# Performance work log

Measured on AMD Instinct MI355X. Metric: run time of the kernel, lower is better.

The kernel has to match this reference:

```python
import jax, jax.numpy as jnp
import numpy as np
from jax import lax

N, L, LQ = 1024, 120, 30
V, D = 50000, 200
POSV, P = 201, 5
H, R = 230, 96
BAG = 8
B = N // BAG
EMB = 3 * D + 2 * P  # 610


def setup_inputs() -> dict:
    key = jax.random.key(0)
    k = jax.random.split(key, 14)
    X = jax.random.randint(k[0], (N, L), 0, V, dtype=jnp.int32)
    Q = jax.random.randint(k[1], (N, LQ), 0, V, dtype=jnp.int32)
    X_Pos1 = jax.random.randint(k[2], (N, L), 0, POSV, dtype=jnp.int32)
    X_Pos2 = jax.random.randint(k[3], (N, L), 0, POSV, dtype=jnp.int32)
    starts = jnp.arange(B, dtype=jnp.int32) * BAG
    X_Scope = jnp.stack([starts, starts + BAG], axis=1)  # [B,2] bag boundaries
    X_Rel = jax.random.randint(k[4], (B,), 0, R, dtype=jnp.int32)
    word_emb = jax.random.normal(k[5], (V, D), jnp.float32) * 0.02
    pos1_emb = jax.random.normal(k[6], (POSV, P), jnp.float32) * 0.02
    pos2_emb = jax.random.normal(k[7], (POSV, P), jnp.float32) * 0.02
    ws_w = jax.random.normal(k[8], (D,), jnp.float32) * 0.05
    wq_w = jax.random.normal(k[9], (D,), jnp.float32) * 0.05
    wsq_w = jax.random.normal(k[10], (D,), jnp.float32) * 0.05
    conv_w = jax.random.normal(k[11], (H, EMB, 3), jnp.float32) * 0.02
    rel_w = jax.random.normal(k[12], (R, H), jnp.float32) * 0.05
    return {
        'X': X, 'Q': Q, 'X_Pos1': X_Pos1, 'X_Pos2': X_Pos2,
        'X_Scope': X_Scope, 'X_Rel': X_Rel,
        'word_emb': word_emb, 'pos1_emb': pos1_emb, 'pos2_emb': pos2_emb,
        'ws_w': ws_w, 'ws_b': jnp.zeros((), jnp.float32),
        'wq_w': wq_w, 'wq_b': jnp.zeros((), jnp.float32),
        'wsq_w': wsq_w, 'wsq_b': jnp.zeros((), jnp.float32),
        'conv_w': conv_w, 'conv_b': jnp.zeros((H,), jnp.float32),
        'rel_w': rel_w, 'rel_b': jnp.zeros((R,), jnp.float32),
    }


def _forward(X, Q, X_Pos1, X_Pos2, X_Scope, X_Rel, word_emb, pos1_emb, pos2_emb,
             ws_w, ws_b, wq_w, wq_b, wsq_w, wsq_b, conv_w, conv_b, rel_w, rel_b):
    s = word_emb[X]            # [N,L,D]
    q = word_emb[Q]            # [N,LQ,D]
    p1 = pos1_emb[X_Pos1]      # [N,L,P]
    p2 = pos2_emb[X_Pos2]
    # ---- qs_att (BiDAF-style), vectorized over the original per-q-position loop ----
    sq = jnp.einsum('nld,nqd,d->nlq', s, q, wsq_w) + wsq_b            # [N,L,LQ]
    h = (s @ ws_w + ws_b)[:, :, None] + (q @ wq_w + wq_b)[:, None, :] + sq
    a = jax.nn.softmax(h, axis=2)
    s2q = jnp.einsum('nlq,nqd->nld', a, q)                            # s2q_att
    bvec = jax.nn.softmax(jnp.max(h, axis=2), axis=1)                 # [N,L]
    q2s = jnp.einsum('nl,nld->nd', bvec, s)[:, None, :]               # [N,1,D]
    x = jnp.concatenate([s, s * s2q, s * q2s], axis=-1)               # [N,L,3D]
    x = jnp.concatenate([x, p1, p2], axis=-1)                         # [N,L,EMB]
    # ---- CNN encoder: conv1d(k=3, same) -> max-over-time -> relu ----
    xc = lax.conv_general_dilated(x.transpose(0, 2, 1), conv_w, (1,), 'SAME',
                                  dimension_numbers=('NCH', 'OIH', 'NCH'))
    xc = xc + conv_b[None, :, None]
    feat = jax.nn.relu(jnp.max(xc, axis=2))                           # [N,H]
    # ---- bag self-attention: per-bag scaled dot-product over sentences ----
    bag_id = jnp.searchsorted(X_Scope[:, 1], jnp.arange(feat.shape[0]), side='right')
    same = bag_id[:, None] == bag_id[None, :]
    scores = (feat @ feat.T) / jnp.sqrt(jnp.float32(feat.shape[-1]))
    scores = jnp.where(same, scores, -1e30)
    feat = jax.nn.softmax(scores, axis=-1) @ feat                     # [N,H]
    # ---- selective attention with gold relation query (segment softmax) ----
    relq = rel_w[X_Rel]                                               # [B,H]
    z = jnp.einsum('nh,nh->n', feat, relq[bag_id])
    m = jax.ops.segment_max(z, bag_id, num_segments=B)
    e = jnp.exp(z - m[bag_id])
    denom = jax.ops.segment_sum(e, bag_id, num_segments=B)
    w = e / denom[bag_id]
    bag_rep = jax.ops.segment_sum(w[:, None] * feat, bag_id, num_segments=B)
    return bag_rep @ rel_w.T + rel_b                                  # [B,R]


def reference(X, Q, X_Pos1, X_Pos2, X_Scope, X_Rel, word_emb, pos1_emb, pos2_emb,
              ws_w, ws_b, wq_w, wq_b, wsq_w, wsq_b, conv_w, conv_b, rel_w, rel_b):
    return _forward(X, Q, X_Pos1, X_Pos2, X_Scope, X_Rel, word_emb, pos1_emb, pos2_emb,
                    ws_w, ws_b, wq_w, wq_b, wsq_w, wsq_b, conv_w, conv_b, rel_w, rel_b)
```

## Files before the change

### kernel.cpp

```cpp
#include <hip/hip_runtime.h>
#include <hip/hip_bf16.h>

#define N_    1024
#define L_    120
#define LQ_   30
#define D_    200
#define P_    5
#define H_    230
#define R_    96
#define BAG_  8
#define B_    128
#define EMB_  610
#define SROWS 130
#define SSTR  232
#define XSTR  40
#define NCH   21

typedef __hip_bfloat16 bf16;
typedef __attribute__((ext_vector_type(8))) short short8;
typedef __attribute__((ext_vector_type(4))) short short4_;
typedef __attribute__((ext_vector_type(4))) float f32x4;

__device__ __forceinline__ float wred_sum64(float v) {
#pragma unroll
  for (int m = 32; m; m >>= 1) v += __shfl_xor(v, m, 64);
  return v;
}
__device__ __forceinline__ float wred_max64(float v) {
#pragma unroll
  for (int m = 32; m; m >>= 1) v = fmaxf(v, __shfl_xor(v, m, 64));
  return v;
}
__device__ __forceinline__ short f2b(float f) {
  bf16 h = __float2bfloat16(f);
  return __builtin_bit_cast(short, h);
}
__device__ __forceinline__ float b2f(bf16 h) { return __bfloat162float(h); }

__global__ __launch_bounds__(256) void k0_prep_w(
    const float* __restrict__ conv_w, bf16* __restrict__ wt)
{
  const int idx = blockIdx.x * 256 + threadIdx.x;
  int e = idx & 7, lane = (idx >> 3) & 63;
  int fid = idx >> 9;
  int ni = fid & 15, cb = (fid >> 4) % NCH, k = fid / (NCH * 16);
  int h = ni * 16 + (lane & 15);
  int ccl = ((lane >> 4) << 3) + e;
  float v = 0.f;
  if (h < H_) {
    int emb_c = -1;
    if (cb < 7) {
      int d = cb * 32 + ccl;
      if (d < D_) emb_c = d;
    } else if (cb < 20) {
      int t = cb - 7;
      int d = 16 * t + (ccl & 15);
      if (d < D_) emb_c = (ccl < 16) ? (D_ + d) : (2 * D_ + d);
    } else if (ccl < 2 * P_) {
      emb_c = 3 * D_ + ccl;
    }
    if (emb_c >= 0) v = conv_w[(size_t)h * (EMB_ * 3) + emb_c * 3 + k];
  }
  wt[idx] = __float2bfloat16(v);
}

__global__ __launch_bounds__(512, 2) void kf_fused(
    const int* __restrict__ X, const int* __restrict__ Q,
    const int* __restrict__ P1, const int* __restrict__ P2,
    const float* __restrict__ word_emb,
    const float* __restrict__ pos1_emb, const float* __restrict__ pos2_emb,
    const float* __restrict__ ws_w, const float* __restrict__ ws_b,
    const float* __restrict__ wq_w, const float* __restrict__ wq_b,
    const float* __restrict__ wsq_w,
    const bf16* __restrict__ wt, const float* __restrict__ conv_b,
    float* __restrict__ feat)
{
  const int n = blockIdx.x;
  const int tid = threadIdx.x;
  const int w = tid >> 6, lane = tid & 63;
  const int g = lane >> 4, c = lane & 15;
  const int wm = w >> 2, wn = w & 3;

  __shared__ __align__(16) bf16 s_lds[SROWS][SSTR];
  __shared__ __align__(16) bf16 qT[208][40];
  __shared__ __align__(16) bf16 a_bf[128][40];
  __shared__ __align__(16) bf16 xstage[3][SROWS][XSTR];
  __shared__ __align__(16) bf16 pos_lds[L_][10];
  __shared__ float hred[8][64];
  __shared__ float wsv[D_], wqv[D_], wsqv[D_];
  __shared__ float sdot[128], qdot[32], hmax[128], bvec[L_];
  __shared__ float q2p[2][D_];
  __shared__ int xidxs[L_], qidxs[LQ_];

  bf16 (*qsw)[SSTR] = (bf16(*)[SSTR])xstage;

  {
    const int4 z4 = {0, 0, 0, 0};
    for (int t = tid; t < SROWS * SSTR * 2 / 16; t += 512) ((int4*)s_lds)[t] = z4;
    for (int t = tid; t < 208 * 40 * 2 / 16;     t += 512) ((int4*)qT)[t] = z4;
    for (int t = tid; t < 32 * SSTR * 2 / 16;    t += 512) ((int4*)qsw)[t] = z4;
  }
  if (tid < 2) qdot[30 + tid] = 0.f;
  if (tid >= 120 && tid < 128) sdot[tid] = 0.f;
  for (int t = tid; t < D_; t += 512) { wsv[t] = ws_w[t]; wqv[t] = wq_w[t]; wsqv[t] = wsq_w[t]; }
  if (tid < L_) xidxs[tid] = X[n * L_ + tid];
  else if (tid >= 128 && tid < 128 + LQ_) qidxs[tid - 128] = Q[n * LQ_ + (tid - 128)];
  __syncthreads();

  const float wsb = ws_b[0], wqb = wq_b[0];

#pragma unroll 5
  for (int l = w; l < L_; l += 8) {
    const int idx = xidxs[l];
    if (lane < 50) {
      const int d = lane * 4;
      float4 v = *(const float4*)(word_emb + (size_t)idx * D_ + d);
      short4_ pk; pk.x = f2b(v.x); pk.y = f2b(v.y); pk.z = f2b(v.z); pk.w = f2b(v.w);
      *(short4_*)&s_lds[1 + l][d] = pk;
    }
  }
  for (int e = tid; e < L_ * 10; e += 512) {
    int r = e / 10, p = e % 10;
    float v = (p < P_) ? pos1_emb[(size_t)P1[n * L_ + r] * P_ + p]
                       : pos2_emb[(size_t)P2[n * L_ + r] * P_ + (p - P_)];
    pos_lds[r][p] = __float2bfloat16(v);
  }
  for (int j = w; j < LQ_; j += 8) {
    const int idx = qidxs[j];
    float part = 0.f;
    if (lane < 50) {
      const int d = lane * 4;
      float4 v = *(const float4*)(word_emb + (size_t)idx * D_ + d);
      part = v.x * wqv[d] + v.y * wqv[d + 1] + v.z * wqv[d + 2] + v.w * wqv[d + 3];
      short4_ pk;
      pk.x = f2b(v.x * wsqv[d]);     pk.y = f2b(v.y * wsqv[d + 1]);
      pk.z = f2b(v.z * wsqv[d + 2]); pk.w = f2b(v.w * wsqv[d + 3]);
      *(short4_*)&qsw[j][d] = pk;
      qT[d][j]     = __float2bfloat16(v.x);
      qT[d + 1][j] = __float2bfloat16(v.y);
      qT[d + 2][j] = __float2bfloat16(v.z);
      qT[d + 3][j] = __float2bfloat16(v.w);
    }
    float sum = wred_sum64(part);
    if (lane == 0) qdot[j] = sum + wqb;
  }
  __syncthreads();

  if (tid < 480) {
    const int r = tid >> 2, base = (tid & 3) * 50;
    float a = 0.f;
#pragma unroll 5
    for (int i = 0; i < 50; i += 2) {
      a += b2f(s_lds[1 + r][base + i]) * wsv[base + i];
      a += b2f(s_lds[1 + r][base + i + 1]) * wsv[base + i + 1];
    }
    a += __shfl_xor(a, 1, 64);
    a += __shfl_xor(a, 2, 64);
    if ((tid & 3) == 0) sdot[r] = a + wsb;
  }
  __syncthreads();

  {
    f32x4 acc0 = {0.f, 0.f, 0.f, 0.f}, acc1 = {0.f, 0.f, 0.f, 0.f};
#pragma unroll
    for (int kk = 0; kk < 7; ++kk) {
      short8 af = *(const short8*)&s_lds[1 + 16 * w + c][kk * 32 + g * 8];
      short8 b0 = *(const short8*)&qsw[c][kk * 32 + g * 8];
      short8 b1 = *(const short8*)&qsw[16 + c][kk * 32 + g * 8];
      acc0 = __builtin_amdgcn_mfma_f32_16x16x32_bf16(af, b0, acc0, 0, 0, 0);
      acc1 = __builtin_amdgcn_mfma_f32_16x16x32_bf16(af, b1, acc1, 0, 0, 0);
    }
    const int rbase = 16 * w + 4 * g;
    const float qd0 = qdot[c], qd1 = qdot[16 + c];
#pragma unroll
    for (int reg = 0; reg < 4; ++reg) {
      const int r = rbase + reg;
      const float s0 = sdot[r];
      float h0 = acc0[reg] + s0 + qd0;
      float h1 = (c < 14) ? (acc1[reg] + s0 + qd1) : -1e30f;
      float m = fmaxf(h0, h1);
#pragma unroll
      for (int msk = 1; msk < 16; msk <<= 1) m = fmaxf(m, __shfl_xor(m, msk, 64));
      float e0 = expf(h0 - m);
      float e1 = (c < 14) ? expf(h1 - m) : 0.f;
      float ssum = e0 + e1;
#pragma unroll
      for (int msk = 1; msk < 16; msk <<= 1) ssum += __shfl_xor(ssum, msk, 64);
      float inv = 1.f / ssum;
      a_bf[r][c]      = __float2bfloat16(e0 * inv);
      a_bf[r][16 + c] = __float2bfloat16(e1 * inv);
      if (c == 0) hmax[r] = m;
    }
  }
  __syncthreads();

  if (w == 0) {
    float v0 = hmax[lane];
    float v1 = (lane < L_ - 64) ? hmax[64 + lane] : -1e30f;
    float m = wred_max64(fmaxf(v0, v1));
    float e0 = expf(v0 - m);
    float e1 = (lane < L_ - 64) ? expf(v1 - m) : 0.f;
    float inv = 1.f / wred_sum64(e0 + e1);
    bvec[lane] = e0 * inv;
    if (lane < L_ - 64) bvec[64 + lane] = e1 * inv;
  } else {
    const int4 z4 = {0, 0, 0, 0};
    for (int t = tid - 64; t < 3 * SROWS * XSTR * 2 / 16; t += 448) ((int4*)xstage)[t] = z4;
  }
  __syncthreads();
  {
    const int d = tid & 255, half = tid >> 8;
    if (d < D_) {
      const int lb = half * 60;
      float a0 = 0.f, a1 = 0.f, a2 = 0.f, a3 = 0.f;
      for (int l = 0; l < 60; l += 4) {
        a0 += bvec[lb + l]     * b2f(s_lds[1 + lb + l][d]);
        a1 += bvec[lb + l + 1] * b2f(s_lds[1 + lb + l + 1][d]);
        a2 += bvec[lb + l + 2] * b2f(s_lds[1 + lb + l + 2][d]);
        a3 += bvec[lb + l + 3] * b2f(s_lds[1 + lb + l + 3][d]);
      }
      q2p[half][d] = (a0 + a1) + (a2 + a3);
    }
  }
  __syncthreads();

  const short* wts = (const short*)wt;
  const short8 aft = *(const short8*)&a_bf[16 * w + c][g * 8];

  auto STAGE = [&](int t, bf16 (*buf)[XSTR]) {
    if (t < 13) {
      short8 bfr = *(const short8*)&qT[t * 16 + c][g * 8];
      f32x4 o = __builtin_amdgcn_mfma_f32_16x16x32_bf16(aft, bfr, (f32x4){0.f,0.f,0.f,0.f}, 0, 0, 0);
#pragma unroll
      for (int reg = 0; reg < 4; ++reg) {
        const int r = 16 * w + 4 * g + reg;
        if (r < L_) {
          float sv = b2f(s_lds[1 + r][t * 16 + c]);
          buf[1 + r][c] = __float2bfloat16(sv * o[reg]);
        }
      }
#pragma unroll
      for (int e = tid; e < L_ * 16; e += 512) {
        const int r = e >> 4, cc = e & 15, dd = t * 16 + cc;
        float v = (dd < D_) ? b2f(s_lds[1 + r][dd]) * (q2p[0][dd] + q2p[1][dd]) : 0.f;
        buf[1 + r][16 + cc] = __float2bfloat16(v);
      }
    } else {
#pragma unroll
      for (int e = tid; e < SROWS * 32; e += 512) {
        const int r = e >> 5, cc = e & 31;
        bf16 v = __float2bfloat16(0.f);
        if (r >= 1 && r <= L_ && cc < 2 * P_) v = pos_lds[r - 1][cc];
        buf[r][cc] = v;
      }
    }
  };

  f32x4 acc[4][4];
#pragma unroll
  for (int i = 0; i < 4; ++i)
#pragma unroll
    for (int j = 0; j < 4; ++j) acc[i][j] = (f32x4){0.f, 0.f, 0.f, 0.f};

  STAGE(0, xstage[0]);

  for (int t = 0; t < 14; ++t) {
    short8 bw[3][4];
#pragma unroll
    for (int k = 0; k < 3; ++k)
#pragma unroll
      for (int ni = 0; ni < 4; ++ni)
        bw[k][ni] = *(const short8*)(
            wts + (((size_t)((k * NCH + 7 + t) * 16 + wn * 4 + ni)) << 9) + lane * 8);

    if (t < 13) STAGE(t + 1, xstage[(t + 1) % 3]);

    if (t < 7) {
      short8 af[3][4];
#pragma unroll
      for (int k = 0; k < 3; ++k)
#pragma unroll
        for (int mi = 0; mi < 4; ++mi)
          af[k][mi] = *(const short8*)&s_lds[wm * 64 + mi * 16 + c + k][t * 32 + g * 8];
#pragma unroll
      for (int k = 0; k < 3; ++k)
#pragma unroll
        for (int ni = 0; ni < 4; ++ni) {
          const short8 b1 = *(const short8*)(
              wts + (((size_t)((k * NCH + t) * 16 + wn * 4 + ni)) << 9) + lane * 8);
#pragma unroll
          for (int mi = 0; mi < 4; ++mi)
            acc[mi][ni] = __builtin_amdgcn_mfma_f32_16x16x32_bf16(af[k][mi], b1, acc[mi][ni], 0, 0, 0);
        }
    }
    __syncthreads();

    {
      bf16 (*buf)[XSTR] = xstage[t % 3];
      short8 afx[3][4];
#pragma unroll
      for (int k = 0; k < 3; ++k)
#pragma unroll
        for (int mi = 0; mi < 4; ++mi)
          afx[k][mi] = *(const short8*)&buf[wm * 64 + mi * 16 + c + k][g * 8];
#pragma unroll
      for (int k = 0; k < 3; ++k)
#pragma unroll
        for (int ni = 0; ni < 4; ++ni)
#pragma unroll
          for (int mi = 0; mi < 4; ++mi)
            acc[mi][ni] = __builtin_amdgcn_mfma_f32_16x16x32_bf16(afx[k][mi], bw[k][ni], acc[mi][ni], 0, 0, 0);
    }
  }

  const int pbase = wm * 64 + (g << 2);
#pragma unroll
  for (int ni = 0; ni < 4; ++ni) {
    float m = -1e30f;
#pragma unroll
    for (int mi = 0; mi < 4; ++mi)
#pragma unroll
      for (int reg = 0; reg < 4; ++reg) {
        int pos = pbase + mi * 16 + reg;
        if (pos < L_) m = fmaxf(m, acc[mi][ni][reg]);
      }
    m = fmaxf(m, __shfl_xor(m, 16, 64));
    m = fmaxf(m, __shfl_xor(m, 32, 64));
    if (g == 0) hred[w][ni * 16 + c] = m;
  }
  __syncthreads();
  for (int h = tid; h < H_; h += 512) {
    int wn2 = h >> 6, hl = h & 63;
    float m = fmaxf(hred[wn2][hl], hred[wn2 + 4][hl]);
    feat[(size_t)n * H_ + h] = fmaxf(0.f, m + conv_b[h]);
  }
}

__global__ __launch_bounds__(256) void k3_bag(
    const float* __restrict__ feat, const int* __restrict__ X_Rel,
    const float* __restrict__ rel_w, const float* __restrict__ rel_b,
    float* __restrict__ out)
{
  const int b = blockIdx.x;
  const int tid = threadIdx.x;
  __shared__ float f[BAG_][231];
  __shared__ float f2[BAG_][231];
  __shared__ float sc[BAG_][BAG_];
  __shared__ float relq[H_];
  __shared__ float zred[BAG_];
  __shared__ float wsel[BAG_];
  __shared__ float brep[H_];

  for (int t = tid; t < BAG_ * H_; t += 256) {
    int i = t / H_, h = t % H_;
    f[i][h] = feat[(size_t)(b * BAG_ + i) * H_ + h];
  }
  const int rel = X_Rel[b];
  for (int t = tid; t < H_; t += 256) relq[t] = rel_w[(size_t)rel * H_ + t];
  __syncthreads();

  if (tid < BAG_ * BAG_) {
    int i = tid >> 3, j = tid & 7;
    float acc = 0.f;
    for (int h = 0; h < H_; ++h) acc += f[i][h] * f[j][h];
    sc[i][j] = acc * (1.0f / sqrtf((float)H_));
  }
  __syncthreads();
  if (tid < BAG_) {
    float m = -1e30f;
    for (int j = 0; j < BAG_; ++j) m = fmaxf(m, sc[tid][j]);
    float s = 0.f;
    for (int j = 0; j < BAG_; ++j) { float e = expf(sc[tid][j] - m); sc[tid][j] = e; s += e; }
    float inv = 1.0f / s;
    for (int j = 0; j < BAG_; ++j) sc[tid][j] *= inv;
  }
  __syncthreads();
  for (int t = tid; t < BAG_ * H_; t += 256) {
    int i = t / H_, h = t % H_;
    float acc = 0.f;
#pragma unroll
    for (int j = 0; j < BAG_; ++j) acc += sc[i][j] * f[j][h];
    f2[i][h] = acc;
  }
  __syncthreads();
  if (tid < BAG_) {
    float acc = 0.f;
    for (int h = 0; h < H_; ++h) acc += f2[tid][h] * relq[h];
    zred[tid] = acc;
  }
  __syncthreads();
  if (tid == 0) {
    float m = -1e30f;
    for (int i = 0; i < BAG_; ++i) m = fmaxf(m, zred[i]);
    float s = 0.f;
    for (int i = 0; i < BAG_; ++i) { float e = expf(zred[i] - m); wsel[i] = e; s += e; }
    float inv = 1.0f / s;
    for (int i = 0; i < BAG_; ++i) wsel[i] *= inv;
  }
  __syncthreads();
  for (int t = tid; t < H_; t += 256) {
    float acc = 0.f;
#pragma unroll
    for (int i = 0; i < BAG_; ++i) acc += wsel[i] * f2[i][t];
    brep[t] = acc;
  }
  __syncthreads();
  if (tid < R_) {
    float acc = 0.f;
    for (int h = 0; h < H_; ++h) acc += brep[h] * rel_w[(size_t)tid * H_ + h];
    out[(size_t)b * R_ + tid] = acc + rel_b[tid];
  }
}

extern "C" void kernel_launch(void* const* d_in, const int* in_sizes, int n_in,
                              void* d_out, int out_size, void* d_ws, size_t ws_size,
                              hipStream_t stream)
{
  const int*   X        = (const int*)d_in[0];
  const int*   Q        = (const int*)d_in[1];
  const int*   P1       = (const int*)d_in[2];
  const int*   P2       = (const int*)d_in[3];
  const int*   X_Rel    = (const int*)d_in[5];
  const float* word_emb = (const float*)d_in[6];
  const float* pos1_emb = (const float*)d_in[7];
  const float* pos2_emb = (const float*)d_in[8];
  const float* ws_w     = (const float*)d_in[9];
  const float* ws_b     = (const float*)d_in[10];
  const float* wq_w     = (const float*)d_in[11];
  const float* wq_b     = (const float*)d_in[12];
  const float* wsq_w    = (const float*)d_in[13];
  const float* conv_w   = (const float*)d_in[15];
  const float* conv_b   = (const float*)d_in[16];
  const float* rel_w    = (const float*)d_in[17];
  const float* rel_b    = (const float*)d_in[18];

  const size_t feat_bytes = ((size_t)N_ * H_ * sizeof(float) + 255) & ~(size_t)255;
  float* feat = (float*)d_ws;
  bf16*  wt   = (bf16*)((char*)d_ws + feat_bytes);

  const int wt_elems = 3 * NCH * 16 * 64 * 8;
  k0_prep_w<<<wt_elems / 256, 256, 0, stream>>>(conv_w, wt);
  kf_fused<<<N_, 512, 0, stream>>>(X, Q, P1, P2, word_emb, pos1_emb, pos2_emb,
                                   ws_w, ws_b, wq_w, wq_b, wsq_w, wt, conv_b, feat);
  k3_bag<<<B_, 256, 0, stream>>>(feat, X_Rel, rel_w, rel_b, (float*)d_out);
}
```

Measured before the change: 233.1 us.

## Double block to 1024 threads and restructure conv GEMM into paired chunk stages

The fused kernel now launches 1024 threads per block (16 waves) instead of 512 with two blocks per CU. The conv MFMA tiling changes from a 2x4 wave grid with 4 N-tiles each to a 2x8 grid with 2 N-tiles. Staging of the attention-derived x-chunks now prepares two chunks per iteration (one per wave-row half) into a wider double buffer, replacing the triple-buffered one-chunk pipeline. The sdot dot-product runs concurrently with the first MFMA phase on the spare waves. Intent is more waves per block and fewer barriers per chunk, at the cost of losing two-blocks-per-CU overlap and raising register pressure per thread.

```diff
diff --git a/kernel.cpp b/kernel.cpp
--- a/kernel.cpp
+++ b/kernel.cpp
@@ -13,7 +13,7 @@
 #define EMB_  610
 #define SROWS 130
 #define SSTR  232
-#define XSTR  40
+#define XSTR  72
 #define NCH   21
 
 typedef __hip_bfloat16 bf16;
@@ -64,7 +64,7 @@
   wt[idx] = __float2bfloat16(v);
 }
 
-__global__ __launch_bounds__(512, 2) void kf_fused(
+__global__ __launch_bounds__(1024, 1) void kf_fused(
     const int* __restrict__ X, const int* __restrict__ Q,
     const int* __restrict__ P1, const int* __restrict__ P2,
     const float* __restrict__ word_emb,
@@ -79,38 +79,39 @@
   const int tid = threadIdx.x;
   const int w = tid >> 6, lane = tid & 63;
   const int g = lane >> 4, c = lane & 15;
-  const int wm = w >> 2, wn = w & 3;
+  const int wm = w >> 3;
+  const int wn = w & 7;
+  const int w8 = w & 7;
 
   __shared__ __align__(16) bf16 s_lds[SROWS][SSTR];
   __shared__ __align__(16) bf16 qT[208][40];
   __shared__ __align__(16) bf16 a_bf[128][40];
-  __shared__ __align__(16) bf16 xstage[3][SROWS][XSTR];
+  __shared__ __align__(16) bf16 xstage[2][SROWS][XSTR];
   __shared__ __align__(16) bf16 pos_lds[L_][10];
-  __shared__ float hred[8][64];
+  __shared__ float hred[16][32];
   __shared__ float wsv[D_], wqv[D_], wsqv[D_];
   __shared__ float sdot[128], qdot[32], hmax[128], bvec[L_];
-  __shared__ float q2p[2][D_];
+  __shared__ float q2p[4][D_];
   __shared__ int xidxs[L_], qidxs[LQ_];
 
-  bf16 (*qsw)[SSTR] = (bf16(*)[SSTR])xstage;
+  bf16 (*qsw)[SSTR] = (bf16(*)[SSTR])&xstage[0][0][0];
 
   {
     const int4 z4 = {0, 0, 0, 0};
-    for (int t = tid; t < SROWS * SSTR * 2 / 16; t += 512) ((int4*)s_lds)[t] = z4;
-    for (int t = tid; t < 208 * 40 * 2 / 16;     t += 512) ((int4*)qT)[t] = z4;
-    for (int t = tid; t < 32 * SSTR * 2 / 16;    t += 512) ((int4*)qsw)[t] = z4;
+    for (int t = tid; t < SROWS * SSTR * 2 / 16; t += 1024) ((int4*)s_lds)[t] = z4;
+    for (int t = tid; t < 208 * 40 * 2 / 16;     t += 1024) ((int4*)qT)[t] = z4;
+    for (int t = tid; t < 32 * SSTR * 2 / 16;    t += 1024) ((int4*)qsw)[t] = z4;
   }
   if (tid < 2) qdot[30 + tid] = 0.f;
   if (tid >= 120 && tid < 128) sdot[tid] = 0.f;
-  for (int t = tid; t < D_; t += 512) { wsv[t] = ws_w[t]; wqv[t] = wq_w[t]; wsqv[t] = wsq_w[t]; }
+  for (int t = tid; t < D_; t += 1024) { wsv[t] = ws_w[t]; wqv[t] = wq_w[t]; wsqv[t] = wsq_w[t]; }
   if (tid < L_) xidxs[tid] = X[n * L_ + tid];
   else if (tid >= 128 && tid < 128 + LQ_) qidxs[tid - 128] = Q[n * LQ_ + (tid - 128)];
   __syncthreads();
 
   const float wsb = ws_b[0], wqb = wq_b[0];
 
-#pragma unroll 5
-  for (int l = w; l < L_; l += 8) {
+  for (int l = w; l < L_; l += 16) {
     const int idx = xidxs[l];
     if (lane < 50) {
       const int d = lane * 4;
@@ -119,13 +120,13 @@
       *(short4_*)&s_lds[1 + l][d] = pk;
     }
   }
-  for (int e = tid; e < L_ * 10; e += 512) {
+  for (int e = tid; e < L_ * 10; e += 1024) {
     int r = e / 10, p = e % 10;
     float v = (p < P_) ? pos1_emb[(size_t)P1[n * L_ + r] * P_ + p]
                        : pos2_emb[(size_t)P2[n * L_ + r] * P_ + (p - P_)];
     pos_lds[r][p] = __float2bfloat16(v);
   }
-  for (int j = w; j < LQ_; j += 8) {
+  for (int j = w; j < LQ_; j += 16) {
     const int idx = qidxs[j];
     float part = 0.f;
     if (lane < 50) {
@@ -146,22 +147,8 @@
   }
   __syncthreads();
 
-  if (tid < 480) {
-    const int r = tid >> 2, base = (tid & 3) * 50;
-    float a = 0.f;
-#pragma unroll 5
-    for (int i = 0; i < 50; i += 2) {
-      a += b2f(s_lds[1 + r][base + i]) * wsv[base + i];
-      a += b2f(s_lds[1 + r][base + i + 1]) * wsv[base + i + 1];
-    }
-    a += __shfl_xor(a, 1, 64);
-    a += __shfl_xor(a, 2, 64);
-    if ((tid & 3) == 0) sdot[r] = a + wsb;
-  }
-  __syncthreads();
-
-  {
-    f32x4 acc0 = {0.f, 0.f, 0.f, 0.f}, acc1 = {0.f, 0.f, 0.f, 0.f};
+  f32x4 acc0 = {0.f, 0.f, 0.f, 0.f}, acc1 = {0.f, 0.f, 0.f, 0.f};
+  if (w < 8) {
 #pragma unroll
     for (int kk = 0; kk < 7; ++kk) {
       short8 af = *(const short8*)&s_lds[1 + 16 * w + c][kk * 32 + g * 8];
@@ -170,6 +157,24 @@
       acc0 = __builtin_amdgcn_mfma_f32_16x16x32_bf16(af, b0, acc0, 0, 0, 0);
       acc1 = __builtin_amdgcn_mfma_f32_16x16x32_bf16(af, b1, acc1, 0, 0, 0);
     }
+  } else {
+    const int idx = tid - 512;
+    if (idx < 480) {
+      const int r = idx >> 2, base = (idx & 3) * 50;
+      float a = 0.f;
+#pragma unroll 5
+      for (int i = 0; i < 50; i += 2) {
+        a += b2f(s_lds[1 + r][base + i]) * wsv[base + i];
+        a += b2f(s_lds[1 + r][base + i + 1]) * wsv[base + i + 1];
+      }
+      a += __shfl_xor(a, 1, 64);
+      a += __shfl_xor(a, 2, 64);
+      if ((idx & 3) == 0) sdot[r] = a + wsb;
+    }
+  }
+  __syncthreads();
+
+  if (w < 8) {
     const int rbase = 16 * w + 4 * g;
     const float qd0 = qdot[c], qd1 = qdot[16 + c];
 #pragma unroll
@@ -191,6 +196,9 @@
       a_bf[r][16 + c] = __float2bfloat16(e1 * inv);
       if (c == 0) hmax[r] = m;
     }
+  } else {
+    const int4 z4 = {0, 0, 0, 0};
+    for (int t = tid - 512; t < 2 * SROWS * XSTR * 2 / 16; t += 512) ((int4*)xstage)[t] = z4;
   }
   __syncthreads();
 
@@ -203,119 +211,112 @@
     float inv = 1.f / wred_sum64(e0 + e1);
     bvec[lane] = e0 * inv;
     if (lane < L_ - 64) bvec[64 + lane] = e1 * inv;
-  } else {
-    const int4 z4 = {0, 0, 0, 0};
-    for (int t = tid - 64; t < 3 * SROWS * XSTR * 2 / 16; t += 448) ((int4*)xstage)[t] = z4;
-  }
-  __syncthreads();
+  }
+  __syncthreads();
+
   {
-    const int d = tid & 255, half = tid >> 8;
+    const int d = tid & 255, quarter = tid >> 8;
     if (d < D_) {
-      const int lb = half * 60;
-      float a0 = 0.f, a1 = 0.f, a2 = 0.f, a3 = 0.f;
-      for (int l = 0; l < 60; l += 4) {
+      const int lb = quarter * 30;
+      float a0 = 0.f, a1 = 0.f;
+      for (int l = 0; l < 30; l += 2) {
         a0 += bvec[lb + l]     * b2f(s_lds[1 + lb + l][d]);
         a1 += bvec[lb + l + 1] * b2f(s_lds[1 + lb + l + 1][d]);
-        a2 += bvec[lb + l + 2] * b2f(s_lds[1 + lb + l + 2][d]);
-        a3 += bvec[lb + l + 3] * b2f(s_lds[1 + lb + l + 3][d]);
-      }
-      q2p[half][d] = (a0 + a1) + (a2 + a3);
+      }
+      q2p[quarter][d] = a0 + a1;
     }
   }
   __syncthreads();
 
   const short* wts = (const short*)wt;
-  const short8 aft = *(const short8*)&a_bf[16 * w + c][g * 8];
-
-  auto STAGE = [&](int t, bf16 (*buf)[XSTR]) {
-    if (t < 13) {
-      short8 bfr = *(const short8*)&qT[t * 16 + c][g * 8];
-      f32x4 o = __builtin_amdgcn_mfma_f32_16x16x32_bf16(aft, bfr, (f32x4){0.f,0.f,0.f,0.f}, 0, 0, 0);
-#pragma unroll
-      for (int reg = 0; reg < 4; ++reg) {
-        const int r = 16 * w + 4 * g + reg;
-        if (r < L_) {
-          float sv = b2f(s_lds[1 + r][t * 16 + c]);
-          buf[1 + r][c] = __float2bfloat16(sv * o[reg]);
+  const short8 aft = *(const short8*)&a_bf[16 * w8 + c][g * 8];
+
+  f32x4 acc[4][2];
+#pragma unroll
+  for (int i = 0; i < 4; ++i) {
+    acc[i][0] = (f32x4){0.f, 0.f, 0.f, 0.f};
+    acc[i][1] = (f32x4){0.f, 0.f, 0.f, 0.f};
+  }
+
+  for (int p = 0; p < 7; ++p) {
+    short8 bw[2][3][2];
+#pragma unroll
+    for (int s2 = 0; s2 < 2; ++s2) {
+      const int t = 2 * p + s2;
+      const int cb = (t < 13) ? (7 + t) : 20;
+#pragma unroll
+      for (int k = 0; k < 3; ++k)
+#pragma unroll
+        for (int ni = 0; ni < 2; ++ni)
+          bw[s2][k][ni] = *(const short8*)(
+              wts + (((size_t)((k * NCH + cb) * 16 + wn * 2 + ni)) << 9) + lane * 8);
+    }
+
+    {
+      const int t = 2 * p + wm;
+      bf16 (*buf)[XSTR] = xstage[p & 1];
+      if (t < 13) {
+        short8 bfr = *(const short8*)&qT[t * 16 + c][g * 8];
+        f32x4 o = __builtin_amdgcn_mfma_f32_16x16x32_bf16(aft, bfr, (f32x4){0.f,0.f,0.f,0.f}, 0, 0, 0);
+#pragma unroll
+        for (int reg = 0; reg < 4; ++reg) {
+          const int r = 16 * w8 + 4 * g + reg;
+          if (r < L_) {
+            float sv = b2f(s_lds[1 + r][t * 16 + c]);
+            buf[1 + r][(t & 1) * 32 + c] = __float2bfloat16(sv * o[reg]);
+          }
         }
-      }
-#pragma unroll
-      for (int e = tid; e < L_ * 16; e += 512) {
-        const int r = e >> 4, cc = e & 15, dd = t * 16 + cc;
-        float v = (dd < D_) ? b2f(s_lds[1 + r][dd]) * (q2p[0][dd] + q2p[1][dd]) : 0.f;
-        buf[1 + r][16 + cc] = __float2bfloat16(v);
-      }
-    } else {
-#pragma unroll
-      for (int e = tid; e < SROWS * 32; e += 512) {
-        const int r = e >> 5, cc = e & 31;
-        bf16 v = __float2bfloat16(0.f);
-        if (r >= 1 && r <= L_ && cc < 2 * P_) v = pos_lds[r - 1][cc];
-        buf[r][cc] = v;
-      }
-    }
-  };
-
-  f32x4 acc[4][4];
-#pragma unroll
-  for (int i = 0; i < 4; ++i)
-#pragma unroll
-    for (int j = 0; j < 4; ++j) acc[i][j] = (f32x4){0.f, 0.f, 0.f, 0.f};
-
-  STAGE(0, xstage[0]);
-
-  for (int t = 0; t < 14; ++t) {
-    short8 bw[3][4];
-#pragma unroll
-    for (int k = 0; k < 3; ++k)
-#pragma unroll
-      for (int ni = 0; ni < 4; ++ni)
-        bw[k][ni] = *(const short8*)(
-            wts + (((size_t)((k * NCH + 7 + t) * 16 + wn * 4 + ni)) << 9) + lane * 8);
-
-    if (t < 13) STAGE(t + 1, xstage[(t + 1) % 3]);
-
-    if (t < 7) {
-      short8 af[3][4];
-#pragma unroll
-      for (int k = 0; k < 3; ++k)
-#pragma unroll
-        for (int mi = 0; mi < 4; ++mi)
-          af[k][mi] = *(const short8*)&s_lds[wm * 64 + mi * 16 + c + k][t * 32 + g * 8];
-#pragma unroll
-      for (int k = 0; k < 3; ++k)
-#pragma unroll
-        for (int ni = 0; ni < 4; ++ni) {
-          const short8 b1 = *(const short8*)(
-              wts + (((size_t)((k * NCH + t) * 16 + wn * 4 + ni)) << 9) + lane * 8);
-#pragma unroll
-          for (int mi = 0; mi < 4; ++mi)
-            acc[mi][ni] = __builtin_amdgcn_mfma_f32_16x16x32_bf16(af[k][mi], b1, acc[mi][ni], 0, 0, 0);
+        for (int e = tid & 511; e < L_ * 16; e += 512) {
+          const int row = e >> 4, cc = e & 15, dd = t * 16 + cc;
+          float v = (dd < D_)
+              ? b2f(s_lds[1 + row][dd]) * (q2p[0][dd] + q2p[1][dd] + q2p[2][dd] + q2p[3][dd])
+              : 0.f;
+          buf[1 + row][(t & 1) * 32 + 16 + cc] = __float2bfloat16(v);
         }
+      } else {
+        for (int e = tid & 511; e < SROWS * 32; e += 512) {
+          const int r = e >> 5, cc = e & 31;
+          bf16 v = __float2bfloat16(0.f);
+          if (r >= 1 && r <= L_ && cc < 2 * P_) v = pos_lds[r - 1][cc];
+          buf[r][32 + cc] = v;
+        }
+      }
+    }
+
+#pragma unroll
+    for (int k = 0; k < 3; ++k) {
+      short8 bx0 = *(const short8*)(
+          wts + (((size_t)((k * NCH + p) * 16 + wn * 2 + 0)) << 9) + lane * 8);
+      short8 bx1 = *(const short8*)(
+          wts + (((size_t)((k * NCH + p) * 16 + wn * 2 + 1)) << 9) + lane * 8);
+#pragma unroll
+      for (int mi = 0; mi < 4; ++mi) {
+        short8 af = *(const short8*)&s_lds[wm * 64 + mi * 16 + c + k][p * 32 + g * 8];
+        acc[mi][0] = __builtin_amdgcn_mfma_f32_16x16x32_bf16(af, bx0, acc[mi][0], 0, 0, 0);
+        acc[mi][1] = __builtin_amdgcn_mfma_f32_16x16x32_bf16(af, bx1, acc[mi][1], 0, 0, 0);
+      }
     }
     __syncthreads();
 
     {
-      bf16 (*buf)[XSTR] = xstage[t % 3];
-      short8 afx[3][4];
-#pragma unroll
-      for (int k = 0; k < 3; ++k)
-#pragma unroll
-        for (int mi = 0; mi < 4; ++mi)
-          afx[k][mi] = *(const short8*)&buf[wm * 64 + mi * 16 + c + k][g * 8];
-#pragma unroll
-      for (int k = 0; k < 3; ++k)
-#pragma unroll
-        for (int ni = 0; ni < 4; ++ni)
-#pragma unroll
-          for (int mi = 0; mi < 4; ++mi)
-            acc[mi][ni] = __builtin_amdgcn_mfma_f32_16x16x32_bf16(afx[k][mi], bw[k][ni], acc[mi][ni], 0, 0, 0);
+      bf16 (*buf)[XSTR] = xstage[p & 1];
+#pragma unroll
+      for (int s2 = 0; s2 < 2; ++s2) {
+#pragma unroll
+        for (int k = 0; k < 3; ++k)
+#pragma unroll
+          for (int mi = 0; mi < 4; ++mi) {
+            short8 afx = *(const short8*)&buf[wm * 64 + mi * 16 + c + k][s2 * 32 + g * 8];
+            acc[mi][0] = __builtin_amdgcn_mfma_f32_16x16x32_bf16(afx, bw[s2][k][0], acc[mi][0], 0, 0, 0);
+            acc[mi][1] = __builtin_amdgcn_mfma_f32_16x16x32_bf16(afx, bw[s2][k][1], acc[mi][1], 0, 0, 0);
+          }
+      }
     }
   }
 
   const int pbase = wm * 64 + (g << 2);
 #pragma unroll
-  for (int ni = 0; ni < 4; ++ni) {
+  for (int ni = 0; ni < 2; ++ni) {
     float m = -1e30f;
 #pragma unroll
     for (int mi = 0; mi < 4; ++mi)
@@ -329,10 +330,10 @@
     if (g == 0) hred[w][ni * 16 + c] = m;
   }
   __syncthreads();
-  for (int h = tid; h < H_; h += 512) {
-    int wn2 = h >> 6, hl = h & 63;
-    float m = fmaxf(hred[wn2][hl], hred[wn2 + 4][hl]);
-    feat[(size_t)n * H_ + h] = fmaxf(0.f, m + conv_b[h]);
+  if (tid < H_) {
+    const int wn2 = tid >> 5, x = tid & 31;
+    float m = fmaxf(hred[wn2][x], hred[8 + wn2][x]);
+    feat[(size_t)n * H_ + tid] = fmaxf(0.f, m + conv_b[tid]);
   }
 }
 
@@ -440,7 +441,7 @@
 
   const int wt_elems = 3 * NCH * 16 * 64 * 8;
   k0_prep_w<<<wt_elems / 256, 256, 0, stream>>>(conv_w, wt);
-  kf_fused<<<N_, 512, 0, stream>>>(X, Q, P1, P2, word_emb, pos1_emb, pos2_emb,
-                                   ws_w, ws_b, wq_w, wq_b, wsq_w, wt, conv_b, feat);
+  kf_fused<<<N_, 1024, 0, stream>>>(X, Q, P1, P2, word_emb, pos1_emb, pos2_emb,
+                                    ws_w, ws_b, wq_w, wq_b, wsq_w, wt, conv_b, feat);
   k3_bag<<<B_, 256, 0, stream>>>(feat, X_Rel, rel_w, rel_b, (float*)d_out);
 }
```

After: 242.7 us. 1.04x slower.
